# Performance work log

Hardware: AMD Instinct MI355X
Metric: run time of the kernel (lower is better)

Reference implementation:

```python
import jax, jax.numpy as jnp
import numpy as np

TEMPERATURE = 0.1  # opt['temperature']; _get_gate returns 0.0 so out_feat == q_feat


def setup_inputs() -> dict:
    key = jax.random.key(0)
    k1, k2 = jax.random.split(key)
    feat = jax.random.normal(k1, (8, 64, 56, 56), dtype=jnp.float32)
    codebook = jax.random.normal(k2, (2048, 64), dtype=jnp.float32)
    return {"feat": feat, "codebook": codebook, "cur_iter": 0}


def reference(feat, codebook, cur_iter):
    b, c, h, w = feat.shape
    k = codebook.shape[0]
    # (b,c,h,w) -> (b*h*w, c)
    flat = jnp.transpose(feat, (0, 2, 3, 1)).reshape(-1, c)
    # squared euclidean distance via norms + matmul: (N, K)
    distance = (jnp.sum(flat * flat, axis=1, keepdims=True)
                + jnp.sum(codebook * codebook, axis=1)
                - 2.0 * jnp.matmul(flat, codebook.T))
    prob = jax.nn.softmax(-distance / TEMPERATURE, axis=1)  # (N, K)
    assignment = jnp.transpose(prob.reshape(b, h, w, k), (0, 3, 1, 2))  # (b,K,h,w)
    q_feat = jnp.matmul(prob, codebook)  # (N, c)
    q_feat = jnp.transpose(q_feat.reshape(b, h, w, c), (0, 3, 1, 2))  # (b,c,h,w)
    # gate = 0.0 -> out_feat = q_feat
    out_feat = q_feat
    # argmin bookkeeping (vq0_update histogram), runs when cur_iter % 25 == 0
    encoding_indices = jnp.argmin(distance, axis=1)  # (N,)
    vq0_update = jax.ops.segment_sum(
        jnp.ones_like(encoding_indices, dtype=jnp.float32),
        encoding_indices, num_segments=k)
    return out_feat, assignment, distance, vq0_update
```

## Files before the change

kernel.cpp:

```cpp
#include <hip/hip_runtime.h>
#include <stddef.h>

#define K_CB   2048
#define C_DIM  64
#define HW_DIM 3136
#define B_DIM  8
#define TR     16

static const size_t OUT_FEAT_SZ = (size_t)B_DIM * C_DIM * HW_DIM;
static const size_t ASSIGN_SZ   = (size_t)B_DIM * K_CB * HW_DIM;
static const size_t DIST_SZ     = (size_t)B_DIM * HW_DIM * K_CB;

__global__ __launch_bounds__(256) void vq_prep(const float* __restrict__ cb,
                                               float* __restrict__ cbT,
                                               float* __restrict__ cnorm,
                                               float* __restrict__ vq0,
                                               float4* __restrict__ outf4) {
    const int t = threadIdx.x, bid = blockIdx.x;
    if (bid < 8) {
        const int k = bid * 256 + t;
        const float4* row = reinterpret_cast<const float4*>(cb + (size_t)k * C_DIM);
        float n = 0.f;
#pragma unroll
        for (int i = 0; i < 16; ++i) {
            float4 v = row[i];
            n = fmaf(v.x, v.x, n); n = fmaf(v.y, v.y, n);
            n = fmaf(v.z, v.z, n); n = fmaf(v.w, v.w, n);
            cbT[(size_t)(4 * i + 0) * K_CB + k] = v.x;
            cbT[(size_t)(4 * i + 1) * K_CB + k] = v.y;
            cbT[(size_t)(4 * i + 2) * K_CB + k] = v.z;
            cbT[(size_t)(4 * i + 3) * K_CB + k] = v.w;
        }
        cnorm[k] = n;
        vq0[k] = 0.f;
    }
    const float4 z = {0.f, 0.f, 0.f, 0.f};
    const size_t nf4 = OUT_FEAT_SZ / 4;
    size_t idx = (size_t)bid * 256 + t;
#pragma unroll
    for (int i = 0; i < 4; ++i) {
        if (idx < nf4) outf4[idx] = z;
        idx += 102400;
    }
}

__global__ __launch_bounds__(512, 2) void vq_main(const float* __restrict__ feat,
                                                  const float* __restrict__ cbT,
                                                  const float* __restrict__ cnorm,
                                                  float* __restrict__ dist,
                                                  float* __restrict__ assign,
                                                  float* __restrict__ vq0) {
    const int t   = threadIdx.x;
    const int n0  = blockIdx.x * TR;
    const int b   = n0 / HW_DIM;
    const int hw0 = n0 % HW_DIM;

    __shared__ float flatT[C_DIM][TR];
    __shared__ float fnorm_s[TR];
    __shared__ float m_s[TR];
    __shared__ float zinv_s[TR];
    __shared__ unsigned long long redmin[TR][8];
    __shared__ float redsum[TR][8];

#pragma unroll
    for (int i = 0; i < 2; ++i) {
        int idx = t + 512 * i;
        int c = idx >> 4, r = idx & 15;
        flatT[c][r] = feat[((size_t)b * C_DIM + c) * HW_DIM + hw0 + r];
    }
    __syncthreads();
    if (t < TR) {
        float s = 0.f;
        for (int c = 0; c < C_DIM; ++c) { float v = flatT[c][t]; s = fmaf(v, v, s); }
        fnorm_s[t] = s;
    }
    __syncthreads();

    float acc[TR][4];
#pragma unroll
    for (int r = 0; r < TR; ++r)
#pragma unroll
        for (int j = 0; j < 4; ++j) acc[r][j] = 0.f;

    for (int c = 0; c < C_DIM; ++c) {
        float cw[4];
#pragma unroll
        for (int j = 0; j < 4; ++j) cw[j] = cbT[(size_t)c * K_CB + j * 512 + t];
        const float4* fT4 = reinterpret_cast<const float4*>(&flatT[c][0]);
        float4 f0 = fT4[0], f1 = fT4[1], f2 = fT4[2], f3 = fT4[3];
        const float fr[TR] = {f0.x, f0.y, f0.z, f0.w, f1.x, f1.y, f1.z, f1.w,
                              f2.x, f2.y, f2.z, f2.w, f3.x, f3.y, f3.z, f3.w};
#pragma unroll
        for (int r = 0; r < TR; ++r)
#pragma unroll
            for (int j = 0; j < 4; ++j) acc[r][j] = fmaf(fr[r], cw[j], acc[r][j]);
    }

    float cn[4];
#pragma unroll
    for (int j = 0; j < 4; ++j) cn[j] = cnorm[j * 512 + t];

    const int lane = t & 63;
    const int wid  = t >> 6;

#pragma unroll
    for (int r = 0; r < TR; ++r) {
        const float fn = fnorm_s[r];
        unsigned long long best = ~0ull;
        float* drow = dist + (size_t)(n0 + r) * K_CB + t;
#pragma unroll
        for (int j = 0; j < 4; ++j) {
            float d = fn + cn[j] - 2.f * acc[r][j];
            acc[r][j] = d;
            drow[j * 512] = d;
            unsigned long long key =
                ((unsigned long long)__float_as_uint(d) << 32) | (unsigned)(j * 512 + t);
            best = key < best ? key : best;
        }
#pragma unroll
        for (int msk = 1; msk < 64; msk <<= 1) {
            unsigned long long o = __shfl_xor(best, msk, 64);
            best = o < best ? o : best;
        }
        if (lane == 0) redmin[r][wid] = best;
    }
    __syncthreads();
    if (t < TR) {
        unsigned long long v = redmin[t][0];
#pragma unroll
        for (int w = 1; w < 8; ++w) { unsigned long long o = redmin[t][w]; v = o < v ? o : v; }
        m_s[t] = __uint_as_float((unsigned)(v >> 32));
        atomicAdd(&vq0[(unsigned)(v & 0xffffffffu)], 1.0f);
    }
    __syncthreads();

#pragma unroll
    for (int r = 0; r < TR; ++r) {
        const float m = m_s[r];
        float s = 0.f;
#pragma unroll
        for (int j = 0; j < 4; ++j) {
            float e = __expf((m - acc[r][j]) * 10.0f);
            acc[r][j] = e;
            s += e;
        }
#pragma unroll
        for (int msk = 1; msk < 64; msk <<= 1) s += __shfl_xor(s, msk, 64);
        if (lane == 0) redsum[r][wid] = s;
    }
    __syncthreads();
    if (t < TR) {
        float s = 0.f;
#pragma unroll
        for (int w = 0; w < 8; ++w) s += redsum[t][w];
        zinv_s[t] = 1.0f / s;
    }
    __syncthreads();

    float inv[TR];
#pragma unroll
    for (int r = 0; r < TR; ++r) inv[r] = zinv_s[r];

    const size_t abase = (size_t)b * K_CB * HW_DIM + hw0;
#pragma unroll
    for (int j = 0; j < 4; ++j) {
        const int k = j * 512 + t;
        float4* dst = reinterpret_cast<float4*>(assign + abase + (size_t)k * HW_DIM);
        float4 v0 = { acc[0][j] * inv[0],  acc[1][j] * inv[1],
                      acc[2][j] * inv[2],  acc[3][j] * inv[3]  };
        float4 v1 = { acc[4][j] * inv[4],  acc[5][j] * inv[5],
                      acc[6][j] * inv[6],  acc[7][j] * inv[7]  };
        float4 v2 = { acc[8][j] * inv[8],  acc[9][j] * inv[9],
                      acc[10][j] * inv[10], acc[11][j] * inv[11] };
        float4 v3 = { acc[12][j] * inv[12], acc[13][j] * inv[13],
                      acc[14][j] * inv[14], acc[15][j] * inv[15] };
        dst[0] = v0; dst[1] = v1; dst[2] = v2; dst[3] = v3;
    }
}

__global__ __launch_bounds__(256, 4) void vq_qfeat(const float* __restrict__ assign,
                                                   const float* __restrict__ cb,
                                                   float* __restrict__ outf) {
    __shared__ float cb_lds[64][68];
    const int t   = threadIdx.x;
    const int bid = blockIdx.x;
    const int ks  = bid & 1;
    const int ht  = (bid >> 1) % 49;
    const int b   = (bid >> 1) / 49;
    const int hw0 = ht * 64;
    const int hwi = t & 31;
    const int c0  = (t >> 5) * 8;

    float a00 = 0.f, a01 = 0.f, a02 = 0.f, a03 = 0.f;
    float a04 = 0.f, a05 = 0.f, a06 = 0.f, a07 = 0.f;
    float a10 = 0.f, a11 = 0.f, a12 = 0.f, a13 = 0.f;
    float a14 = 0.f, a15 = 0.f, a16 = 0.f, a17 = 0.f;

    const float* ap = assign + (size_t)b * K_CB * HW_DIM + hw0 + hwi;
    const int srow = t >> 2;
    const int scol = (t & 3) * 16;

    for (int kt = 0; kt < 16; ++kt) {
        const int k0 = ks * 1024 + kt * 64;
        const float4* src = reinterpret_cast<const float4*>(cb + (size_t)(k0 + srow) * C_DIM + scol);
        float4* dstl = reinterpret_cast<float4*>(&cb_lds[srow][scol]);
#pragma unroll
        for (int q = 0; q < 4; ++q) dstl[q] = src[q];
        __syncthreads();

#pragma unroll 4
        for (int kk = 0; kk < 64; ++kk) {
            const size_t koff = (size_t)(k0 + kk) * HW_DIM;
            const float p0 = ap[koff];
            const float p1 = ap[koff + 32];
            const float4 v0 = *reinterpret_cast<const float4*>(&cb_lds[kk][c0]);
            const float4 v1 = *reinterpret_cast<const float4*>(&cb_lds[kk][c0 + 4]);
            a00 = fmaf(p0, v0.x, a00); a01 = fmaf(p0, v0.y, a01);
            a02 = fmaf(p0, v0.z, a02); a03 = fmaf(p0, v0.w, a03);
            a04 = fmaf(p0, v1.x, a04); a05 = fmaf(p0, v1.y, a05);
            a06 = fmaf(p0, v1.z, a06); a07 = fmaf(p0, v1.w, a07);
            a10 = fmaf(p1, v0.x, a10); a11 = fmaf(p1, v0.y, a11);
            a12 = fmaf(p1, v0.z, a12); a13 = fmaf(p1, v0.w, a13);
            a14 = fmaf(p1, v1.x, a14); a15 = fmaf(p1, v1.y, a15);
            a16 = fmaf(p1, v1.z, a16); a17 = fmaf(p1, v1.w, a17);
        }
        __syncthreads();
    }

    float* ob = outf + ((size_t)b * C_DIM + c0) * HW_DIM + hw0 + hwi;
    atomicAdd(ob + 0 * HW_DIM,      a00); atomicAdd(ob + 0 * HW_DIM + 32, a10);
    atomicAdd(ob + 1 * HW_DIM,      a01); atomicAdd(ob + 1 * HW_DIM + 32, a11);
    atomicAdd(ob + 2 * HW_DIM,      a02); atomicAdd(ob + 2 * HW_DIM + 32, a12);
    atomicAdd(ob + 3 * HW_DIM,      a03); atomicAdd(ob + 3 * HW_DIM + 32, a13);
    atomicAdd(ob + 4 * HW_DIM,      a04); atomicAdd(ob + 4 * HW_DIM + 32, a14);
    atomicAdd(ob + 5 * HW_DIM,      a05); atomicAdd(ob + 5 * HW_DIM + 32, a15);
    atomicAdd(ob + 6 * HW_DIM,      a06); atomicAdd(ob + 6 * HW_DIM + 32, a16);
    atomicAdd(ob + 7 * HW_DIM,      a07); atomicAdd(ob + 7 * HW_DIM + 32, a17);
}

extern "C" void kernel_launch(void* const* d_in, const int* in_sizes, int n_in,
                              void* d_out, int out_size, void* d_ws, size_t ws_size,
                              hipStream_t stream) {
    const float* feat = (const float*)d_in[0];
    const float* cb   = (const float*)d_in[1];

    float* out      = (float*)d_out;
    float* out_feat = out;
    float* assign   = out + OUT_FEAT_SZ;
    float* dist     = out + OUT_FEAT_SZ + ASSIGN_SZ;
    float* vq0      = out + OUT_FEAT_SZ + ASSIGN_SZ + DIST_SZ;

    float* cbT   = (float*)d_ws;
    float* cnorm = cbT + (size_t)C_DIM * K_CB;

    vq_prep<<<400, 256, 0, stream>>>(cb, cbT, cnorm, vq0, (float4*)out_feat);
    vq_main<<<(B_DIM * HW_DIM) / TR, 512, 0, stream>>>(feat, cbT, cnorm, dist, assign, vq0);
    vq_qfeat<<<B_DIM * (HW_DIM / 64) * 2, 256, 0, stream>>>(assign, cb, out_feat);
}
```

Measured before the change: 824.1 us.

## Vectorize codebook loads, remove split-K atomics and zero-fill in q_feat

The main kernel now gives each thread four consecutive codebook entries, so codebook, norm and distance accesses become float4. The next channel's codebook row is prefetched while the current one is being accumulated. The q_feat kernel drops its two-way K split, so it no longer needs to zero the output in the prep kernel or use atomicAdd. Instead it reads assignment pairs as float2 and writes results with plain float2 stores. In exchange q_feat runs half as many blocks, each with a longer loop, and the occupancy hints are raised, which may cause register spilling in vq_main.

```diff
diff --git a/kernel.cpp b/kernel.cpp
--- a/kernel.cpp
+++ b/kernel.cpp
@@ -14,37 +14,25 @@
 __global__ __launch_bounds__(256) void vq_prep(const float* __restrict__ cb,
                                                float* __restrict__ cbT,
                                                float* __restrict__ cnorm,
-                                               float* __restrict__ vq0,
-                                               float4* __restrict__ outf4) {
-    const int t = threadIdx.x, bid = blockIdx.x;
-    if (bid < 8) {
-        const int k = bid * 256 + t;
-        const float4* row = reinterpret_cast<const float4*>(cb + (size_t)k * C_DIM);
-        float n = 0.f;
-#pragma unroll
-        for (int i = 0; i < 16; ++i) {
-            float4 v = row[i];
-            n = fmaf(v.x, v.x, n); n = fmaf(v.y, v.y, n);
-            n = fmaf(v.z, v.z, n); n = fmaf(v.w, v.w, n);
-            cbT[(size_t)(4 * i + 0) * K_CB + k] = v.x;
-            cbT[(size_t)(4 * i + 1) * K_CB + k] = v.y;
-            cbT[(size_t)(4 * i + 2) * K_CB + k] = v.z;
-            cbT[(size_t)(4 * i + 3) * K_CB + k] = v.w;
-        }
-        cnorm[k] = n;
-        vq0[k] = 0.f;
-    }
-    const float4 z = {0.f, 0.f, 0.f, 0.f};
-    const size_t nf4 = OUT_FEAT_SZ / 4;
-    size_t idx = (size_t)bid * 256 + t;
-#pragma unroll
-    for (int i = 0; i < 4; ++i) {
-        if (idx < nf4) outf4[idx] = z;
-        idx += 102400;
-    }
-}
-
-__global__ __launch_bounds__(512, 2) void vq_main(const float* __restrict__ feat,
+                                               float* __restrict__ vq0) {
+    const int k = blockIdx.x * 256 + threadIdx.x;
+    const float4* row = reinterpret_cast<const float4*>(cb + (size_t)k * C_DIM);
+    float n = 0.f;
+#pragma unroll
+    for (int i = 0; i < 16; ++i) {
+        float4 v = row[i];
+        n = fmaf(v.x, v.x, n); n = fmaf(v.y, v.y, n);
+        n = fmaf(v.z, v.z, n); n = fmaf(v.w, v.w, n);
+        cbT[(size_t)(4 * i + 0) * K_CB + k] = v.x;
+        cbT[(size_t)(4 * i + 1) * K_CB + k] = v.y;
+        cbT[(size_t)(4 * i + 2) * K_CB + k] = v.z;
+        cbT[(size_t)(4 * i + 3) * K_CB + k] = v.w;
+    }
+    cnorm[k] = n;
+    vq0[k] = 0.f;
+}
+
+__global__ __launch_bounds__(512, 4) void vq_main(const float* __restrict__ feat,
                                                   const float* __restrict__ cbT,
                                                   const float* __restrict__ cnorm,
                                                   float* __restrict__ dist,
@@ -82,23 +70,27 @@
 #pragma unroll
         for (int j = 0; j < 4; ++j) acc[r][j] = 0.f;
 
+    const float4* cbT4 = reinterpret_cast<const float4*>(cbT);
+    float4 cwv = cbT4[t];
     for (int c = 0; c < C_DIM; ++c) {
-        float cw[4];
-#pragma unroll
-        for (int j = 0; j < 4; ++j) cw[j] = cbT[(size_t)c * K_CB + j * 512 + t];
+        float4 cwn;
+        if (c < C_DIM - 1) cwn = cbT4[(c + 1) * (K_CB / 4) + t];
         const float4* fT4 = reinterpret_cast<const float4*>(&flatT[c][0]);
         float4 f0 = fT4[0], f1 = fT4[1], f2 = fT4[2], f3 = fT4[3];
         const float fr[TR] = {f0.x, f0.y, f0.z, f0.w, f1.x, f1.y, f1.z, f1.w,
                               f2.x, f2.y, f2.z, f2.w, f3.x, f3.y, f3.z, f3.w};
 #pragma unroll
-        for (int r = 0; r < TR; ++r)
-#pragma unroll
-            for (int j = 0; j < 4; ++j) acc[r][j] = fmaf(fr[r], cw[j], acc[r][j]);
-    }
-
-    float cn[4];
-#pragma unroll
-    for (int j = 0; j < 4; ++j) cn[j] = cnorm[j * 512 + t];
+        for (int r = 0; r < TR; ++r) {
+            acc[r][0] = fmaf(fr[r], cwv.x, acc[r][0]);
+            acc[r][1] = fmaf(fr[r], cwv.y, acc[r][1]);
+            acc[r][2] = fmaf(fr[r], cwv.z, acc[r][2]);
+            acc[r][3] = fmaf(fr[r], cwv.w, acc[r][3]);
+        }
+        cwv = cwn;
+    }
+
+    const float4 cn = reinterpret_cast<const float4*>(cnorm)[t];
+    const float cna[4] = {cn.x, cn.y, cn.z, cn.w};
 
     const int lane = t & 63;
     const int wid  = t >> 6;
@@ -107,14 +99,17 @@
     for (int r = 0; r < TR; ++r) {
         const float fn = fnorm_s[r];
         unsigned long long best = ~0ull;
-        float* drow = dist + (size_t)(n0 + r) * K_CB + t;
+        float d0 = fn + cna[0] - 2.f * acc[r][0];
+        float d1 = fn + cna[1] - 2.f * acc[r][1];
+        float d2 = fn + cna[2] - 2.f * acc[r][2];
+        float d3 = fn + cna[3] - 2.f * acc[r][3];
+        acc[r][0] = d0; acc[r][1] = d1; acc[r][2] = d2; acc[r][3] = d3;
+        float4 dv = {d0, d1, d2, d3};
+        reinterpret_cast<float4*>(dist + (size_t)(n0 + r) * K_CB)[t] = dv;
 #pragma unroll
         for (int j = 0; j < 4; ++j) {
-            float d = fn + cn[j] - 2.f * acc[r][j];
-            acc[r][j] = d;
-            drow[j * 512] = d;
             unsigned long long key =
-                ((unsigned long long)__float_as_uint(d) << 32) | (unsigned)(j * 512 + t);
+                ((unsigned long long)__float_as_uint(acc[r][j]) << 32) | (unsigned)(4 * t + j);
             best = key < best ? key : best;
         }
 #pragma unroll
@@ -164,7 +159,7 @@
     const size_t abase = (size_t)b * K_CB * HW_DIM + hw0;
 #pragma unroll
     for (int j = 0; j < 4; ++j) {
-        const int k = j * 512 + t;
+        const int k = 4 * t + j;
         float4* dst = reinterpret_cast<float4*>(assign + abase + (size_t)k * HW_DIM);
         float4 v0 = { acc[0][j] * inv[0],  acc[1][j] * inv[1],
                       acc[2][j] * inv[2],  acc[3][j] * inv[3]  };
@@ -178,17 +173,16 @@
     }
 }
 
-__global__ __launch_bounds__(256, 4) void vq_qfeat(const float* __restrict__ assign,
+__global__ __launch_bounds__(256, 8) void vq_qfeat(const float* __restrict__ assign,
                                                    const float* __restrict__ cb,
                                                    float* __restrict__ outf) {
     __shared__ float cb_lds[64][68];
     const int t   = threadIdx.x;
     const int bid = blockIdx.x;
-    const int ks  = bid & 1;
-    const int ht  = (bid >> 1) % 49;
-    const int b   = (bid >> 1) / 49;
+    const int ht  = bid % 49;
+    const int b   = bid / 49;
     const int hw0 = ht * 64;
-    const int hwi = t & 31;
+    const int hwp = (t & 31) * 2;
     const int c0  = (t >> 5) * 8;
 
     float a00 = 0.f, a01 = 0.f, a02 = 0.f, a03 = 0.f;
@@ -196,46 +190,44 @@
     float a10 = 0.f, a11 = 0.f, a12 = 0.f, a13 = 0.f;
     float a14 = 0.f, a15 = 0.f, a16 = 0.f, a17 = 0.f;
 
-    const float* ap = assign + (size_t)b * K_CB * HW_DIM + hw0 + hwi;
+    const float* ap = assign + (size_t)b * K_CB * HW_DIM + hw0 + hwp;
     const int srow = t >> 2;
     const int scol = (t & 3) * 16;
 
-    for (int kt = 0; kt < 16; ++kt) {
-        const int k0 = ks * 1024 + kt * 64;
+    for (int kt = 0; kt < 32; ++kt) {
+        const int k0 = kt * 64;
         const float4* src = reinterpret_cast<const float4*>(cb + (size_t)(k0 + srow) * C_DIM + scol);
         float4* dstl = reinterpret_cast<float4*>(&cb_lds[srow][scol]);
 #pragma unroll
         for (int q = 0; q < 4; ++q) dstl[q] = src[q];
         __syncthreads();
 
-#pragma unroll 4
+#pragma unroll 8
         for (int kk = 0; kk < 64; ++kk) {
-            const size_t koff = (size_t)(k0 + kk) * HW_DIM;
-            const float p0 = ap[koff];
-            const float p1 = ap[koff + 32];
+            const float2 p = *reinterpret_cast<const float2*>(ap + (size_t)(k0 + kk) * HW_DIM);
             const float4 v0 = *reinterpret_cast<const float4*>(&cb_lds[kk][c0]);
             const float4 v1 = *reinterpret_cast<const float4*>(&cb_lds[kk][c0 + 4]);
-            a00 = fmaf(p0, v0.x, a00); a01 = fmaf(p0, v0.y, a01);
-            a02 = fmaf(p0, v0.z, a02); a03 = fmaf(p0, v0.w, a03);
-            a04 = fmaf(p0, v1.x, a04); a05 = fmaf(p0, v1.y, a05);
-            a06 = fmaf(p0, v1.z, a06); a07 = fmaf(p0, v1.w, a07);
-            a10 = fmaf(p1, v0.x, a10); a11 = fmaf(p1, v0.y, a11);
-            a12 = fmaf(p1, v0.z, a12); a13 = fmaf(p1, v0.w, a13);
-            a14 = fmaf(p1, v1.x, a14); a15 = fmaf(p1, v1.y, a15);
-            a16 = fmaf(p1, v1.z, a16); a17 = fmaf(p1, v1.w, a17);
+            a00 = fmaf(p.x, v0.x, a00); a01 = fmaf(p.x, v0.y, a01);
+            a02 = fmaf(p.x, v0.z, a02); a03 = fmaf(p.x, v0.w, a03);
+            a04 = fmaf(p.x, v1.x, a04); a05 = fmaf(p.x, v1.y, a05);
+            a06 = fmaf(p.x, v1.z, a06); a07 = fmaf(p.x, v1.w, a07);
+            a10 = fmaf(p.y, v0.x, a10); a11 = fmaf(p.y, v0.y, a11);
+            a12 = fmaf(p.y, v0.z, a12); a13 = fmaf(p.y, v0.w, a13);
+            a14 = fmaf(p.y, v1.x, a14); a15 = fmaf(p.y, v1.y, a15);
+            a16 = fmaf(p.y, v1.z, a16); a17 = fmaf(p.y, v1.w, a17);
         }
         __syncthreads();
     }
 
-    float* ob = outf + ((size_t)b * C_DIM + c0) * HW_DIM + hw0 + hwi;
-    atomicAdd(ob + 0 * HW_DIM,      a00); atomicAdd(ob + 0 * HW_DIM + 32, a10);
-    atomicAdd(ob + 1 * HW_DIM,      a01); atomicAdd(ob + 1 * HW_DIM + 32, a11);
-    atomicAdd(ob + 2 * HW_DIM,      a02); atomicAdd(ob + 2 * HW_DIM + 32, a12);
-    atomicAdd(ob + 3 * HW_DIM,      a03); atomicAdd(ob + 3 * HW_DIM + 32, a13);
-    atomicAdd(ob + 4 * HW_DIM,      a04); atomicAdd(ob + 4 * HW_DIM + 32, a14);
-    atomicAdd(ob + 5 * HW_DIM,      a05); atomicAdd(ob + 5 * HW_DIM + 32, a15);
-    atomicAdd(ob + 6 * HW_DIM,      a06); atomicAdd(ob + 6 * HW_DIM + 32, a16);
-    atomicAdd(ob + 7 * HW_DIM,      a07); atomicAdd(ob + 7 * HW_DIM + 32, a17);
+    float* ob = outf + ((size_t)b * C_DIM + c0) * HW_DIM + hw0 + hwp;
+    float2 s0 = {a00, a10}; *reinterpret_cast<float2*>(ob + 0 * HW_DIM) = s0;
+    float2 s1 = {a01, a11}; *reinterpret_cast<float2*>(ob + 1 * HW_DIM) = s1;
+    float2 s2 = {a02, a12}; *reinterpret_cast<float2*>(ob + 2 * HW_DIM) = s2;
+    float2 s3 = {a03, a13}; *reinterpret_cast<float2*>(ob + 3 * HW_DIM) = s3;
+    float2 s4 = {a04, a14}; *reinterpret_cast<float2*>(ob + 4 * HW_DIM) = s4;
+    float2 s5 = {a05, a15}; *reinterpret_cast<float2*>(ob + 5 * HW_DIM) = s5;
+    float2 s6 = {a06, a16}; *reinterpret_cast<float2*>(ob + 6 * HW_DIM) = s6;
+    float2 s7 = {a07, a17}; *reinterpret_cast<float2*>(ob + 7 * HW_DIM) = s7;
 }
 
 extern "C" void kernel_launch(void* const* d_in, const int* in_sizes, int n_in,
@@ -253,7 +245,7 @@
     float* cbT   = (float*)d_ws;
     float* cnorm = cbT + (size_t)C_DIM * K_CB;
 
-    vq_prep<<<400, 256, 0, stream>>>(cb, cbT, cnorm, vq0, (float4*)out_feat);
+    vq_prep<<<K_CB / 256, 256, 0, stream>>>(cb, cbT, cnorm, vq0);
     vq_main<<<(B_DIM * HW_DIM) / TR, 512, 0, stream>>>(feat, cbT, cnorm, dist, assign, vq0);
-    vq_qfeat<<<B_DIM * (HW_DIM / 64) * 2, 256, 0, stream>>>(assign, cb, out_feat);
-}
+    vq_qfeat<<<B_DIM * (HW_DIM / 64), 256, 0, stream>>>(assign, cb, out_feat);
+}
```

Result: slower. 1.559 ms (+89.1%).
